# Optimization experiments

Measured on AMD Instinct MI355X. Metric: run time of the kernel, lower is better.

Reference implementation:

```python
import jax, jax.numpy as jnp
import numpy as np
from jax import lax

B, T, D, H, O = 64, 2048, 512, 512, 512


def setup_inputs() -> dict:
    key = jax.random.key(0)
    ks = jax.random.split(key, 8)
    s_in = 1.0 / np.sqrt(D)
    s_h = 1.0 / np.sqrt(H)
    s_o = 1.0 / np.sqrt(O)
    return {
        "embeddings": jax.random.normal(ks[0], (B, T, D), dtype=jnp.float32),
        "last_logits": jax.random.normal(ks[1], (B, O), dtype=jnp.float32),
        "Whx": jax.random.normal(ks[2], (H, D), dtype=jnp.float32) * s_in,
        "bhx": jax.random.normal(ks[3], (H,), dtype=jnp.float32) * s_in,
        "Wyh": jax.random.normal(ks[4], (H, O), dtype=jnp.float32) * s_o,
        "byh": jax.random.normal(ks[5], (H,), dtype=jnp.float32) * s_o,
        "Wout": jax.random.normal(ks[6], (O, H), dtype=jnp.float32) * s_h,
        "bout": jax.random.normal(ks[7], (O,), dtype=jnp.float32) * s_h,
    }


def reference(embeddings, last_logits, Whx, bhx, Wyh, byh, Wout, bout):
    # Precompute the input projection for all timesteps in one big GEMM:
    # xh[b,t,h] = hx(x_t)  (time-parallel part of the Jordan cell)
    xh = jnp.einsum('btd,hd->bth', embeddings, Whx) + bhx  # [B,T,H]

    def step(y_t, xh_t):
        # h_t = tanh(hx(x_t) + yh(y_t)); y_t = lm_head(h_t)
        h = jnp.tanh(xh_t + y_t @ Wyh.T + byh)   # [B,H]
        y = h @ Wout.T + bout                    # [B,O]
        return y, y

    last, ys = lax.scan(step, last_logits, jnp.swapaxes(xh, 0, 1))  # scan over T
    logits = jnp.swapaxes(ys, 0, 1)  # [B,T,O]
    return logits, last
```

## Files before the change

kernel.cpp:

```cpp
#include <hip/hip_runtime.h>
#include <hip/hip_bf16.h>


#define NB 64
#define NT 2048
#define ND 512
#define NH 512
#define NO 512
#define TH (NT * NH)

typedef float f32x4 __attribute__((ext_vector_type(4)));
typedef __bf16 bf16x8 __attribute__((ext_vector_type(8)));
typedef unsigned short u16x8 __attribute__((ext_vector_type(8)));
typedef unsigned short u16x4 __attribute__((ext_vector_type(4)));

__device__ __forceinline__ unsigned short f2bf(float x) {
  unsigned u = __builtin_bit_cast(unsigned, x);
  u += 0x7FFFu + ((u >> 16) & 1u);
  return (unsigned short)(u >> 16);
}
__device__ __forceinline__ float bf2f(unsigned short u) {
  return __builtin_bit_cast(float, (unsigned)u << 16);
}
__device__ __forceinline__ bf16x8 ld_frag(const unsigned short* p) {
  u16x8 r = *(const u16x8*)p;
  return __builtin_bit_cast(bf16x8, r);
}
__device__ __forceinline__ f32x4 ld_frag4(const unsigned short* p) {
  return *(const f32x4*)p;
}
__device__ __forceinline__ float fast_tanh(float x) {
  float ax = __builtin_fabsf(x);
  float e = __builtin_amdgcn_exp2f(ax * 2.8853900817779268f);
  float r = 1.0f - 2.0f * __builtin_amdgcn_rcpf(e + 1.0f);
  return __builtin_copysignf(r, x);
}


__global__ void k_bias(const float* __restrict__ Wyh, const float* __restrict__ bout,
                       const float* __restrict__ bhx, const float* __restrict__ byh,
                       float* bias_t0, float* bias_t) {
  int j = threadIdx.x;
  const float* row = Wyh + j * NO;
  float acc = 0.f;
  for (int o = 0; o < NO; ++o) acc += row[o] * bout[o];
  bias_t0[j] = bhx[j] + byh[j];
  bias_t[j]  = bhx[j] + byh[j] + acc;
}

__global__ void k_z0(const float* __restrict__ ll, const float* __restrict__ Wyh,
                     float* z0) {
  int b = blockIdx.x, j = threadIdx.x;
  const float* row = Wyh + j * NO;
  const float* lr = ll + b * NO;
  float acc = 0.f;
  for (int o = 0; o < NO; ++o) acc += lr[o] * row[o];
  z0[b * NH + j] = acc;
}

__global__ void k_wc(const float* __restrict__ Wyh, const float* __restrict__ Wout,
                     float* Wc) {
  int j = blockIdx.x, k = threadIdx.x;
  float acc = 0.f;
  for (int o = 0; o < NO; ++o) acc += Wyh[j * NO + o] * Wout[o * NH + k];
  Wc[j * NH + k] = acc;
}

__global__ void k_frag(const float* __restrict__ src, unsigned short* __restrict__ dst) {
  int gid = blockIdx.x * 256 + threadIdx.x;
  int lane = gid & 63, tidx = gid >> 6;
  int nt = tidx & 31, kt = tidx >> 5;
  const float* s = src + (size_t)(nt * 16 + (lane & 15)) * 512 + kt * 32 + (lane >> 4) * 8;
  unsigned short* d = dst + (size_t)gid * 8;
#pragma unroll
  for (int i = 0; i < 8; ++i) d[i] = f2bf(s[i]);
}

__device__ __forceinline__ int pre_idx(int col) {
  int w = col >> 7;
  return w * 128 + ((w >> 1) << 9) + (col & 15) * 8 + ((col >> 4) & 7);
}

template <int MODE>
__global__ __launch_bounds__(512) void k_gemm(
    const void* __restrict__ Ain, const unsigned short* __restrict__ fragB,
    float* __restrict__ out, const float* __restrict__ bias_t0,
    const float* __restrict__ bias_t, const float* __restrict__ z0,
    const float* __restrict__ bout, float* __restrict__ last) {
  __shared__ __align__(16) unsigned short a_lds[64 * 512];
  int tid = threadIdx.x;
  long bt0 = (long)blockIdx.x * 64;

  if (MODE == 0) {
    const float* A = (const float*)Ain;
#pragma unroll
    for (int it = 0; it < 16; ++it) {
      int chunk = it * 512 + tid;
      int r = chunk >> 7, c4 = chunk & 127;
      float4 v = ((const float4*)A)[(bt0 + r) * 128 + c4];
      int idx = (r * 512 + c4 * 4) ^ ((r & 7) << 3);
      unsigned short* p = &a_lds[idx];
      p[0] = f2bf(v.x); p[1] = f2bf(v.y); p[2] = f2bf(v.z); p[3] = f2bf(v.w);
    }
  } else {
    const unsigned short* A = (const unsigned short*)Ain;
#pragma unroll
    for (int it = 0; it < 8; ++it) {
      int chunk = it * 512 + tid;
      int r = chunk >> 6, c8 = chunk & 63;
      u16x8 v = *(const u16x8*)(A + (size_t)(bt0 + r) * 1024 + 256 + c8 * 8);
      int idx = (r * 512 + c8 * 8) ^ ((r & 7) << 3);
      *(u16x8*)&a_lds[idx] = v;
    }
  }
  __syncthreads();

  int wave = tid >> 6, lane = tid & 63;
  int r0 = (wave & 3) * 16, c0 = (wave >> 2) * 256;
  f32x4 acc[16];
#pragma unroll
  for (int n = 0; n < 16; ++n) acc[n] = (f32x4){0.f, 0.f, 0.f, 0.f};
  int arow = r0 + (lane & 15);

  for (int kt = 0; kt < 16; ++kt) {
    int aidx = (arow * 512 + kt * 32 + (lane >> 4) * 8) ^ ((arow & 7) << 3);
    bf16x8 a = ld_frag(&a_lds[aidx]);
    const unsigned short* bp = fragB + ((size_t)(kt * 32 + (c0 >> 4)) * 64 + lane) * 8;
#pragma unroll
    for (int n = 0; n < 16; ++n) {
      bf16x8 b = ld_frag(bp + (size_t)n * 512);
      acc[n] = __builtin_amdgcn_mfma_f32_16x16x32_bf16(a, b, acc[n], 0, 0, 0);
    }
  }

#pragma unroll
  for (int n = 0; n < 16; ++n) {
    int col = c0 + n * 16 + (lane & 15);
#pragma unroll
    for (int reg = 0; reg < 4; ++reg) {
      long row = bt0 + r0 + (lane >> 4) * 4 + reg;
      float v = acc[n][reg];
      if (MODE == 0) {
        int t = (int)(row & (NT - 1));
        long b = row >> 11;
        v += (t == 0) ? (bias_t0[col] + z0[b * NH + col]) : bias_t[col];
        ((unsigned short*)out)[row * 1024 + pre_idx(col)] = f2bf(v);
      } else {
        v += bout[col];
        out[row * 512 + col] = v;
        if ((row & (NT - 1)) == NT - 1) last[(row >> 11) * 512 + col] = v;
      }
    }
  }
}

__global__ __launch_bounds__(512, 2) void k_scan(float* __restrict__ buf,
                                                 const unsigned short* __restrict__ fragWc) {
  __shared__ __align__(16) unsigned short h_lds[2][16 * 512];
  __shared__ __align__(16) unsigned short wc_lds[8 * 12 * 512];
  unsigned short* hbuf = (unsigned short*)buf;
  const int tid = threadIdx.x;
  const int b0 = blockIdx.x * 16;
  const int wave = tid >> 6, lane = tid & 63;
  const int arow = lane & 15, bb = lane >> 4;
  const int c0 = wave * 64;
  const int swz = (arow & 7) << 3;
  const int w2 = wave >> 1;
  const int poff = w2 * 128 + ((w2 >> 1) << 9) + arow * 8 + (wave & 1) * 4;

  const unsigned short* bW = fragWc + ((size_t)(wave * 4) * 64 + lane) * 8;

#pragma unroll
  for (int g = 0; g < 3; ++g)
#pragma unroll
    for (int n = 0; n < 4; ++n) {
      f32x4 v = ld_frag4(bW + (size_t)((13 + g) * 32 + n) * 512);
      *(f32x4*)&wc_lds[(size_t)((wave * 3 + g) * 4 + n) * 512 + lane * 8] = v;
    }

  f32x4 ba[7][4];
#pragma unroll
  for (int g = 0; g < 7; ++g)
#pragma unroll
    for (int n = 0; n < 4; ++n) ba[g][n] = ld_frag4(bW + (size_t)(g * 32 + n) * 512);
#pragma unroll
  for (int g = 0; g < 7; ++g)
#pragma unroll
    for (int n = 0; n < 4; ++n) asm volatile("" : "+a"(ba[g][n]));

  u16x4 pr[4];
#pragma unroll
  for (int r = 0; r < 4; ++r)
    pr[r] = *(const u16x4*)(hbuf + (size_t)(b0 + bb * 4 + r) * (size_t)(NT * 1024) + poff);
#pragma unroll
  for (int r = 0; r < 4; ++r)
#pragma unroll
    for (int n = 0; n < 4; ++n) {
      float h = fast_tanh(bf2f(pr[r][n]));
      int b = bb * 4 + r, col = c0 + n * 16 + arow;
      h_lds[0][(b * 512 + col) ^ ((b & 7) << 3)] = f2bf(h);
    }

  const unsigned short* pPre[4];
#pragma unroll
  for (int r = 0; r < 4; ++r)
    pPre[r] = hbuf + (size_t)(b0 + bb * 4 + r) * (size_t)(NT * 1024) + 1024 + poff;
#pragma unroll
  for (int r = 0; r < 4; ++r) pr[r] = *(const u16x4*)pPre[r];

  const int bA = tid >> 6, c8A = tid & 63;
  const int bB = bA + 8;
  const int ldsA = (bA * 512 + c8A * 8) ^ ((bA & 7) << 3);
  const int ldsB = (bB * 512 + c8A * 8) ^ ((bB & 7) << 3);
  unsigned short* pHA =
      hbuf + (size_t)(b0 + bA) * (size_t)(NT * 1024) + 256 + c8A * 8;
  unsigned short* pHB =
      hbuf + (size_t)(b0 + bB) * (size_t)(NT * 1024) + 256 + c8A * 8;

  bf16x8 q0[4], q1[4], q2[4];
#pragma unroll
  for (int n = 0; n < 4; ++n) q0[n] = ld_frag(bW + (size_t)(7 * 32 + n) * 512);
#pragma unroll
  for (int n = 0; n < 4; ++n) q1[n] = ld_frag(bW + (size_t)(8 * 32 + n) * 512);
#pragma unroll
  for (int n = 0; n < 4; ++n) q2[n] = ld_frag(bW + (size_t)(9 * 32 + n) * 512);

  __syncthreads();

#define AIDX(k) ((arow * 512 + (k) * 32 + bb * 8) ^ swz)
#define AGPR_STEP(G)                                                            \
  {                                                                             \
    bf16x8 a = ld_frag(hs + AIDX(G));                                           \
    _Pragma("unroll") for (int n = 0; n < 4; ++n)                               \
        acc[n] = __builtin_amdgcn_mfma_f32_16x16x32_bf16(                       \
            a, __builtin_bit_cast(bf16x8, ba[G][n]), acc[n], 0, 0, 0);          \
  }
#define STREAM_STEP(Q, KT, RKT)                                                 \
  {                                                                             \
    bf16x8 a = ld_frag(hs + AIDX(KT));                                          \
    _Pragma("unroll") for (int n = 0; n < 4; ++n)                               \
        acc[n] = __builtin_amdgcn_mfma_f32_16x16x32_bf16(a, Q[n], acc[n], 0, 0, 0); \
    _Pragma("unroll") for (int n = 0; n < 4; ++n)                               \
        Q[n] = ld_frag(bWs + (size_t)((RKT) * 32 + n) * 512);                   \
  }
#define LDS_STEP(G)                                                             \
  {                                                                             \
    bf16x8 a = ld_frag(hs + AIDX(13 + G));                                      \
    _Pragma("unroll") for (int n = 0; n < 4; ++n) {                             \
      bf16x8 b = ld_frag(&wc_lds[(size_t)((wave * 3 + (G)) * 4 + n) * 512 + lane * 8]); \
      acc[n] = __builtin_amdgcn_mfma_f32_16x16x32_bf16(a, b, acc[n], 0, 0, 0);  \
    }                                                                           \
  }

#pragma unroll 1
  for (int t = 1; t < NT; ++t) {
    const unsigned short* bWs = bW;
    asm volatile("" : "+v"(bWs));

    const unsigned short* hs = h_lds[(t - 1) & 1];

    {
      u16x8 hA = *(const u16x8*)&hs[ldsA];
      u16x8 hB = *(const u16x8*)&hs[ldsB];
      *(u16x8*)pHA = hA;
      *(u16x8*)pHB = hB;
      pHA += 1024; pHB += 1024;
    }

    f32x4 acc[4];
#pragma unroll
    for (int n = 0; n < 4; ++n)
#pragma unroll
      for (int r = 0; r < 4; ++r) acc[n][r] = bf2f(pr[r][n]);

    AGPR_STEP(0) AGPR_STEP(1) AGPR_STEP(2) AGPR_STEP(3)
    AGPR_STEP(4) AGPR_STEP(5) AGPR_STEP(6)
    STREAM_STEP(q0, 7, 10)
    STREAM_STEP(q1, 8, 11)
    STREAM_STEP(q2, 9, 12)
    LDS_STEP(0)
    STREAM_STEP(q0, 10, 7)
    LDS_STEP(1)
    STREAM_STEP(q1, 11, 8)
    LDS_STEP(2)
    STREAM_STEP(q2, 12, 9)

    if (t < NT - 1) {
#pragma unroll
      for (int r = 0; r < 4; ++r) {
        pPre[r] += 1024;
        pr[r] = *(const u16x4*)pPre[r];
      }
    }

    unsigned short* hdst = h_lds[t & 1];
#pragma unroll
    for (int n = 0; n < 4; ++n)
#pragma unroll
      for (int r = 0; r < 4; ++r) {
        int b = bb * 4 + r;
        float h = fast_tanh(acc[n][r]);
        hdst[(b * 512 + c0 + n * 16 + arow) ^ ((b & 7) << 3)] = f2bf(h);
      }

    asm volatile("s_waitcnt lgkmcnt(0)" ::: "memory");
    __builtin_amdgcn_s_barrier();
    asm volatile("" ::: "memory");
  }

  {
    const unsigned short* hs = h_lds[(NT - 1) & 1];
    u16x8 hA = *(const u16x8*)&hs[ldsA];
    u16x8 hB = *(const u16x8*)&hs[ldsB];
    *(u16x8*)pHA = hA;
    *(u16x8*)pHB = hB;
  }
#undef LDS_STEP
#undef STREAM_STEP
#undef AGPR_STEP
#undef AIDX
}

extern "C" void kernel_launch(void* const* d_in, const int* in_sizes, int n_in,
                              void* d_out, int out_size, void* d_ws, size_t ws_size,
                              hipStream_t stream) {
  const float* emb  = (const float*)d_in[0];
  const float* ll   = (const float*)d_in[1];
  const float* Whx  = (const float*)d_in[2];
  const float* bhx  = (const float*)d_in[3];
  const float* Wyh  = (const float*)d_in[4];
  const float* byh  = (const float*)d_in[5];
  const float* Wout = (const float*)d_in[6];
  const float* bout = (const float*)d_in[7];

  float* buf  = (float*)d_out;
  float* last = buf + (size_t)NB * NT * NO;

  char* ws = (char*)d_ws;
  unsigned short* fragWhx  = (unsigned short*)ws;
  unsigned short* fragWc   = (unsigned short*)(ws + (512 * 512 * 2));
  unsigned short* fragWout = (unsigned short*)(ws + 2 * (512 * 512 * 2));
  float* z0      = (float*)(ws + 3 * (512 * 512 * 2));
  float* bias_t0 = z0 + NB * NH;
  float* bias_t  = bias_t0 + NH;
  float* Wc_f32  = bias_t + NH;

  k_bias<<<1, 512, 0, stream>>>(Wyh, bout, bhx, byh, bias_t0, bias_t);
  k_z0<<<64, 512, 0, stream>>>(ll, Wyh, z0);
  k_wc<<<512, 512, 0, stream>>>(Wyh, Wout, Wc_f32);
  k_frag<<<128, 256, 0, stream>>>(Whx, fragWhx);
  k_frag<<<128, 256, 0, stream>>>(Wc_f32, fragWc);
  k_frag<<<128, 256, 0, stream>>>(Wout, fragWout);

  k_gemm<0><<<2048, 512, 0, stream>>>(emb, fragWhx, buf, bias_t0, bias_t, z0, bout, last);
  k_scan<<<4, 512, 0, stream>>>(buf, fragWc);
  k_gemm<1><<<2048, 512, 0, stream>>>(buf, fragWout, buf, bias_t0, bias_t, z0, bout, last);
}
```

Baseline: 7.682 ms.

## Swap MFMA operand roles in scan and stream remaining weights from global

```diff
diff --git a/kernel.cpp b/kernel.cpp
--- a/kernel.cpp
+++ b/kernel.cpp
@@ -77,8 +77,7 @@
 }
 
 __device__ __forceinline__ int pre_idx(int col) {
-  int w = col >> 7;
-  return w * 128 + ((w >> 1) << 9) + (col & 15) * 8 + ((col >> 4) & 7);
+  return (col < 256) ? col : col + 512;
 }
 
 template <int MODE>
@@ -157,27 +156,17 @@
 __global__ __launch_bounds__(512, 2) void k_scan(float* __restrict__ buf,
                                                  const unsigned short* __restrict__ fragWc) {
   __shared__ __align__(16) unsigned short h_lds[2][16 * 512];
-  __shared__ __align__(16) unsigned short wc_lds[8 * 12 * 512];
   unsigned short* hbuf = (unsigned short*)buf;
   const int tid = threadIdx.x;
   const int b0 = blockIdx.x * 16;
   const int wave = tid >> 6, lane = tid & 63;
-  const int arow = lane & 15, bb = lane >> 4;
+  const int bat = lane & 15, bb = lane >> 4;
   const int c0 = wave * 64;
-  const int swz = (arow & 7) << 3;
-  const int w2 = wave >> 1;
-  const int poff = w2 * 128 + ((w2 >> 1) << 9) + arow * 8 + (wave & 1) * 4;
+  const int swz = (bat & 7) << 3;
+  const int j0 = c0 + bb * 4;
 
   const unsigned short* bW = fragWc + ((size_t)(wave * 4) * 64 + lane) * 8;
 
-#pragma unroll
-  for (int g = 0; g < 3; ++g)
-#pragma unroll
-    for (int n = 0; n < 4; ++n) {
-      f32x4 v = ld_frag4(bW + (size_t)((13 + g) * 32 + n) * 512);
-      *(f32x4*)&wc_lds[(size_t)((wave * 3 + g) * 4 + n) * 512 + lane * 8] = v;
-    }
-
   f32x4 ba[7][4];
 #pragma unroll
   for (int g = 0; g < 7; ++g)
@@ -188,25 +177,22 @@
 #pragma unroll
     for (int n = 0; n < 4; ++n) asm volatile("" : "+a"(ba[g][n]));
 
+  const unsigned short* pPre =
+      hbuf + (size_t)(b0 + bat) * (size_t)(NT * 1024) + pre_idx(j0);
   u16x4 pr[4];
 #pragma unroll
-  for (int r = 0; r < 4; ++r)
-    pr[r] = *(const u16x4*)(hbuf + (size_t)(b0 + bb * 4 + r) * (size_t)(NT * 1024) + poff);
-#pragma unroll
-  for (int r = 0; r < 4; ++r)
-#pragma unroll
-    for (int n = 0; n < 4; ++n) {
-      float h = fast_tanh(bf2f(pr[r][n]));
-      int b = bb * 4 + r, col = c0 + n * 16 + arow;
-      h_lds[0][(b * 512 + col) ^ ((b & 7) << 3)] = f2bf(h);
-    }
-
-  const unsigned short* pPre[4];
-#pragma unroll
-  for (int r = 0; r < 4; ++r)
-    pPre[r] = hbuf + (size_t)(b0 + bb * 4 + r) * (size_t)(NT * 1024) + 1024 + poff;
-#pragma unroll
-  for (int r = 0; r < 4; ++r) pr[r] = *(const u16x4*)pPre[r];
+  for (int n = 0; n < 4; ++n) pr[n] = *(const u16x4*)(pPre + n * 16);
+#pragma unroll
+  for (int n = 0; n < 4; ++n) {
+    u16x4 hv;
+#pragma unroll
+    for (int r = 0; r < 4; ++r) hv[r] = f2bf(fast_tanh(bf2f(pr[n][r])));
+    int idx = (bat * 512 + j0 + n * 16) ^ swz;
+    *(u16x4*)&h_lds[0][idx] = hv;
+  }
+  pPre += 1024;
+#pragma unroll
+  for (int n = 0; n < 4; ++n) pr[n] = *(const u16x4*)(pPre + n * 16);
 
   const int bA = tid >> 6, c8A = tid & 63;
   const int bB = bA + 8;
@@ -227,29 +213,21 @@
 
   __syncthreads();
 
-#define AIDX(k) ((arow * 512 + (k) * 32 + bb * 8) ^ swz)
+#define BIDX(k) ((bat * 512 + (k) * 32 + bb * 8) ^ swz)
 #define AGPR_STEP(G)                                                            \
   {                                                                             \
-    bf16x8 a = ld_frag(hs + AIDX(G));                                           \
+    bf16x8 b = ld_frag(hs + BIDX(G));                                           \
     _Pragma("unroll") for (int n = 0; n < 4; ++n)                               \
         acc[n] = __builtin_amdgcn_mfma_f32_16x16x32_bf16(                       \
-            a, __builtin_bit_cast(bf16x8, ba[G][n]), acc[n], 0, 0, 0);          \
+            __builtin_bit_cast(bf16x8, ba[G][n]), b, acc[n], 0, 0, 0);          \
   }
 #define STREAM_STEP(Q, KT, RKT)                                                 \
   {                                                                             \
-    bf16x8 a = ld_frag(hs + AIDX(KT));                                          \
+    bf16x8 b = ld_frag(hs + BIDX(KT));                                          \
     _Pragma("unroll") for (int n = 0; n < 4; ++n)                               \
-        acc[n] = __builtin_amdgcn_mfma_f32_16x16x32_bf16(a, Q[n], acc[n], 0, 0, 0); \
+        acc[n] = __builtin_amdgcn_mfma_f32_16x16x32_bf16(Q[n], b, acc[n], 0, 0, 0); \
     _Pragma("unroll") for (int n = 0; n < 4; ++n)                               \
         Q[n] = ld_frag(bWs + (size_t)((RKT) * 32 + n) * 512);                   \
-  }
-#define LDS_STEP(G)                                                             \
-  {                                                                             \
-    bf16x8 a = ld_frag(hs + AIDX(13 + G));                                      \
-    _Pragma("unroll") for (int n = 0; n < 4; ++n) {                             \
-      bf16x8 b = ld_frag(&wc_lds[(size_t)((wave * 3 + (G)) * 4 + n) * 512 + lane * 8]); \
-      acc[n] = __builtin_amdgcn_mfma_f32_16x16x32_bf16(a, b, acc[n], 0, 0, 0);  \
-    }                                                                           \
   }
 
 #pragma unroll 1
@@ -271,37 +249,35 @@
 #pragma unroll
     for (int n = 0; n < 4; ++n)
 #pragma unroll
-      for (int r = 0; r < 4; ++r) acc[n][r] = bf2f(pr[r][n]);
+      for (int r = 0; r < 4; ++r) acc[n][r] = bf2f(pr[n][r]);
 
     AGPR_STEP(0) AGPR_STEP(1) AGPR_STEP(2) AGPR_STEP(3)
     AGPR_STEP(4) AGPR_STEP(5) AGPR_STEP(6)
     STREAM_STEP(q0, 7, 10)
     STREAM_STEP(q1, 8, 11)
     STREAM_STEP(q2, 9, 12)
-    LDS_STEP(0)
-    STREAM_STEP(q0, 10, 7)
-    LDS_STEP(1)
-    STREAM_STEP(q1, 11, 8)
-    LDS_STEP(2)
-    STREAM_STEP(q2, 12, 9)
+    STREAM_STEP(q0, 10, 13)
+    STREAM_STEP(q1, 11, 14)
+    STREAM_STEP(q2, 12, 15)
+    STREAM_STEP(q0, 13, 7)
+    STREAM_STEP(q1, 14, 8)
+    STREAM_STEP(q2, 15, 9)
 
     if (t < NT - 1) {
-#pragma unroll
-      for (int r = 0; r < 4; ++r) {
-        pPre[r] += 1024;
-        pr[r] = *(const u16x4*)pPre[r];
-      }
+      pPre += 1024;
+#pragma unroll
+      for (int n = 0; n < 4; ++n) pr[n] = *(const u16x4*)(pPre + n * 16);
     }
 
     unsigned short* hdst = h_lds[t & 1];
 #pragma unroll
-    for (int n = 0; n < 4; ++n)
-#pragma unroll
-      for (int r = 0; r < 4; ++r) {
-        int b = bb * 4 + r;
-        float h = fast_tanh(acc[n][r]);
-        hdst[(b * 512 + c0 + n * 16 + arow) ^ ((b & 7) << 3)] = f2bf(h);
-      }
+    for (int n = 0; n < 4; ++n) {
+      u16x4 hv;
+#pragma unroll
+      for (int r = 0; r < 4; ++r) hv[r] = f2bf(fast_tanh(acc[n][r]));
+      int idx = (bat * 512 + j0 + n * 16) ^ swz;
+      *(u16x4*)&hdst[idx] = hv;
+    }
 
     asm volatile("s_waitcnt lgkmcnt(0)" ::: "memory");
     __builtin_amdgcn_s_barrier();
@@ -315,10 +291,9 @@
     *(u16x8*)pHA = hA;
     *(u16x8*)pHB = hB;
   }
-#undef LDS_STEP
 #undef STREAM_STEP
 #undef AGPR_STEP
-#undef AIDX
+#undef BIDX
 }
 
 extern "C" void kernel_launch(void* const* d_in, const int* in_sizes, int n_in,
```

Measured after the change: 9.446 ms. 23.0% more time.
